# Performance work log

Measured on AMD Instinct MI355X. Metric: run time of the kernel, lower is better.

The kernel has to match this reference:

```python
import jax, jax.numpy as jnp
import numpy as np


def setup_inputs() -> dict:
    key = jax.random.key(0)
    k1, k2 = jax.random.split(key)
    N = 8192
    means = jax.random.normal(k1, (N, 3), dtype=jnp.float32) * 2.0
    normals = jax.random.normal(k2, (N, 3), dtype=jnp.float32)
    normals = normals / (jnp.linalg.norm(normals, axis=-1, keepdims=True) + 1e-8)
    return {"means": means, "normals": normals, "k": 8}


def reference(means, normals, k):
    # Pairwise Euclidean distances via the ||a-b||^2 expansion: avoids the
    # N x N x 3 diff tensor the original torch code materializes (same math).
    sq = jnp.sum(means * means, axis=-1)                      # (N,)
    d2 = sq[:, None] + sq[None, :] - 2.0 * (means @ means.T)  # (N, N)
    dists = jnp.sqrt(jnp.maximum(d2, 0.0))
    # k+1 smallest distances (self is the 0-distance nearest); drop self.
    dists = jax.lax.stop_gradient(dists)
    _, idx = jax.lax.top_k(-dists, k + 1)                     # (N, k+1)
    idx = idx[:, 1:]                                          # (N, k)
    neighbors = means[idx]                                    # (N, k, 3)
    local_diff = neighbors - means[:, None, :]                # (N, k, 3)
    plane_dist = jnp.sum(local_diff * normals[:, None, :], axis=-1)  # (N, k)
    return jnp.mean(jnp.abs(plane_dist))
```

## Files before the change

### kernel.cpp

```cpp
#include <hip/hip_runtime.h>
#include <hip/hip_bf16.h>

#define NPTS 8192
#define KNN 8
#define RPB 16
#define STAGES 8
#define SCOLS 1024

typedef __attribute__((ext_vector_type(8))) short bf16x8;
typedef __attribute__((ext_vector_type(4))) float f32x4;

__device__ __forceinline__ unsigned int bf16rne(float v) {
    unsigned int u = __float_as_uint(v);
    return (u + 0x7FFFu + ((u >> 16) & 1u)) >> 16;
}
__device__ __forceinline__ float bf2f(unsigned int h) { return __uint_as_float(h << 16); }

__device__ __forceinline__ void insert8(unsigned int (&best)[KNN], unsigned int key) {
#pragma unroll
    for (int t = 0; t < KNN; ++t) {
        const unsigned int lo = min(best[t], key);
        key = max(best[t], key);
        best[t] = lo;
    }
}
__device__ __forceinline__ void insert4(unsigned int (&b)[4], unsigned int key) {
#pragma unroll
    for (int t = 0; t < 4; ++t) {
        const unsigned int lo = min(b[t], key);
        key = max(b[t], key);
        b[t] = lo;
    }
}

__global__ __launch_bounds__(512) void prep_thresh(const float* __restrict__ means,
                                                   float4* __restrict__ pts,
                                                   uint4* __restrict__ cf0,
                                                   uint4* __restrict__ cf1,
                                                   uint4* __restrict__ rf0,
                                                   uint4* __restrict__ rf1,
                                                   float* __restrict__ Tm_arr,
                                                   float* __restrict__ out) {
    __shared__ unsigned int lds4[16][32][5];
    __shared__ unsigned int lds8[4][32][8];
    const int tid = threadIdx.x;
    const int pl = tid & 31;
    const int cls = tid >> 5;
    const int pt = blockIdx.x * 32 + pl;
    if (blockIdx.x == 0 && tid == 0) out[0] = 0.0f;

    const float x = means[3 * pt + 0];
    const float y = means[3 * pt + 1];
    const float z = means[3 * pt + 2];
    const float sq = x * x + y * y + z * z;
    if (cls == 0) {
        pts[pt] = make_float4(x, y, z, sq);
        const unsigned int hx = bf16rne(x), lx = bf16rne(x - bf2f(hx));
        const unsigned int hy = bf16rne(y), ly = bf16rne(y - bf2f(hy));
        const unsigned int hz = bf16rne(z), lz = bf16rne(z - bf2f(hz));
        const unsigned int hs = bf16rne(sq), ls = bf16rne(sq - bf2f(hs));
        cf0[pt] = make_uint4(hx | (lx << 16), hx | (hy << 16),
                             ly | (hy << 16), hz | (lz << 16));
        cf1[pt] = make_uint4(hz | (hs << 16), ls | (0x3F80u << 16), 0x3F80u, 0u);
        const float ax = -2.0f * x, ay = -2.0f * y, az = -2.0f * z;
        const unsigned int hax = bf16rne(ax), lax = bf16rne(ax - bf2f(hax));
        const unsigned int hay = bf16rne(ay), lay = bf16rne(ay - bf2f(hay));
        const unsigned int haz = bf16rne(az), laz = bf16rne(az - bf2f(haz));
        const unsigned int hsr = bf16rne(sq), lsr = bf16rne(sq - bf2f(hsr));
        rf0[pt] = make_uint4(hax | (hax << 16), lax | (hay << 16),
                             hay | (lay << 16), haz | (haz << 16));
        rf1[pt] = make_uint4(laz | (0x3F80u << 16), 0x3F80u | (hsr << 16), lsr, 0u);
    }

    const float mx2 = -2.0f * x, my2 = -2.0f * y, mz2 = -2.0f * z;
    unsigned int b4[4] = {~0u, ~0u, ~0u, ~0u};
#pragma unroll 4
    for (int m = 0; m < 32; ++m) {
        const int col = 16 * (cls + 16 * m);
        const float qx = means[3 * col + 0];
        const float qy = means[3 * col + 1];
        const float qz = means[3 * col + 2];
        const float qsq = qx * qx + qy * qy + qz * qz;
        const float d2 = fmaxf(fmaf(mx2, qx, fmaf(my2, qy, fmaf(mz2, qz, sq + qsq))), 0.0f);
        unsigned int key = (__float_as_uint(d2) & 0xFFFFE000u) | (unsigned int)col;
        key = (col == pt) ? ~0u : key;
        insert4(b4, key);
    }
#pragma unroll
    for (int j = 0; j < 4; ++j) lds4[cls][pl][j] = b4[j];
    __syncthreads();
    if (tid < 128) {
        const int p2 = tid & 31, q = tid >> 5;
        unsigned int bb[KNN];
#pragma unroll
        for (int s = 0; s < KNN; ++s) bb[s] = ~0u;
        for (int c = q * 4; c < q * 4 + 4; ++c)
#pragma unroll
            for (int j = 0; j < 4; ++j) insert8(bb, lds4[c][p2][j]);
#pragma unroll
        for (int s = 0; s < KNN; ++s) lds8[q][p2][s] = bb[s];
    }
    __syncthreads();
    if (tid < 32) {
        unsigned int bb[KNN];
#pragma unroll
        for (int s = 0; s < KNN; ++s) bb[s] = ~0u;
        for (int q = 0; q < 4; ++q)
#pragma unroll
            for (int s = 0; s < KNN; ++s) insert8(bb, lds8[q][tid][s]);
        const float Tf = __uint_as_float(bb[7] & 0xFFFFE000u);
        Tm_arr[blockIdx.x * 32 + tid] = Tf + 0.02f + 2e-3f * Tf;
    }
}

__global__ __launch_bounds__(512) void mfma_knn(const uint4* __restrict__ cf0,
                                                const uint4* __restrict__ cf1,
                                                const uint4* __restrict__ rf0,
                                                const uint4* __restrict__ rf1,
                                                const float4* __restrict__ pts,
                                                const float* __restrict__ Tm_arr,
                                                const float* __restrict__ normals,
                                                float* __restrict__ out) {
    __shared__ unsigned int lds_acc[8][16][64];
    __shared__ unsigned int km[8][RPB][KNN + 1];
    const int tid = threadIdx.x;
    const int l = tid & 63;
    const int wv = __builtin_amdgcn_readfirstlane(tid >> 6);
    const int R = l & 15;
    const int g = l >> 4;
    const int arow = blockIdx.x * RPB + R;

    const float4 mp = pts[arow];
    const float Tm = Tm_arr[arow];

    uint4 bu = make_uint4(0u, 0u, 0u, 0u);
    if (g == 0) bu = rf0[arow];
    else if (g == 1) bu = rf1[arow];
    union { uint4 u; bf16x8 v; } Bf; Bf.u = bu;
    const f32x4 zero = {0.0f, 0.0f, 0.0f, 0.0f};

    const uint4* __restrict__ asel = (g == 1) ? cf1 : cf0;

    unsigned int best[KNN];
#pragma unroll
    for (int s = 0; s < KNN; ++s) best[s] = ~0u;

#pragma unroll 1
    for (int s = 0; s < STAGES; ++s) {
        const int lbase = s * SCOLS + wv * 128 + R;
        const int cbase = s * SCOLS + wv * 128;
#pragma unroll
        for (int h = 0; h < 2; ++h) {
            unsigned int m = 0u;
#pragma unroll
            for (int mt4 = 0; mt4 < 4; ++mt4) {
                const int mt = h * 4 + mt4;
                union { uint4 u; bf16x8 v; } Af;
                Af.u = asel[lbase + mt * 16];
                const f32x4 acc = __builtin_amdgcn_mfma_f32_16x16x32_bf16(Af.v, Bf.v, zero, 0, 0, 0);
                lds_acc[wv][mt4 * 4 + 0][l] = __float_as_uint(acc[0]);
                lds_acc[wv][mt4 * 4 + 1][l] = __float_as_uint(acc[1]);
                lds_acc[wv][mt4 * 4 + 2][l] = __float_as_uint(acc[2]);
                lds_acc[wv][mt4 * 4 + 3][l] = __float_as_uint(acc[3]);
                m = m + m + ((acc[0] <= Tm) ? 1u : 0u);
                m = m + m + ((acc[1] <= Tm) ? 1u : 0u);
                m = m + m + ((acc[2] <= Tm) ? 1u : 0u);
                m = m + m + ((acc[3] <= Tm) ? 1u : 0u);
            }
            while (m) {
                const int b = __ffs(m) - 1;
                m &= m - 1;
                const int t = 15 - b;
                const float av = fmaxf(__uint_as_float(lds_acc[wv][t][l]), 0.0f);
                const int col = cbase + (h * 4 + (t >> 2)) * 16 + g * 4 + (t & 3);
                unsigned int key = (__float_as_uint(av) & 0xFFFFE000u) | (unsigned int)col;
                key = (col == arow) ? ~0u : key;
                insert8(best, key);
            }
        }
    }

#pragma unroll
    for (int st = 16; st <= 32; st <<= 1) {
        unsigned int tk[KNN];
#pragma unroll
        for (int s = 0; s < KNN; ++s) tk[s] = __shfl_xor(best[s], st);
#pragma unroll
        for (int s = 0; s < KNN; ++s) insert8(best, tk[s]);
    }
    if (l < RPB) {
#pragma unroll
        for (int s = 0; s < KNN; ++s) km[wv][l][s] = best[s];
    }
    for (int st = 1; st < 8; st <<= 1) {
        __syncthreads();
        if (((wv & (2 * st - 1)) == 0) && l < RPB) {
#pragma unroll
            for (int s = 0; s < KNN; ++s) insert8(best, km[wv + st][l][s]);
#pragma unroll
            for (int s = 0; s < KNN; ++s) km[wv][l][s] = best[s];
        }
    }

    if (wv == 0) {
        float sum = 0.0f;
        if (l < RPB) {
            const float nx = normals[3 * arow + 0];
            const float ny = normals[3 * arow + 1];
            const float nz = normals[3 * arow + 2];
#pragma unroll
            for (int s = 0; s < KNN; ++s) {
                const int nbr = (int)(best[s] & 0x1FFFu);
                const float4 q = pts[nbr];
                sum += fabsf((q.x - mp.x) * nx + (q.y - mp.y) * ny + (q.z - mp.z) * nz);
            }
        }
#pragma unroll
        for (int off = 8; off > 0; off >>= 1) sum += __shfl_down(sum, off);
        if (l == 0) atomicAdd(out, sum * (1.0f / ((float)NPTS * (float)KNN)));
    }
}

extern "C" void kernel_launch(void* const* d_in, const int* in_sizes, int n_in,
                              void* d_out, int out_size, void* d_ws, size_t ws_size,
                              hipStream_t stream) {
    const float* means = (const float*)d_in[0];
    const float* normals = (const float*)d_in[1];
    float* out = (float*)d_out;
    char* ws = (char*)d_ws;
    uint4* cf0 = (uint4*)ws;
    uint4* cf1 = (uint4*)(ws + 131072);
    uint4* rf0 = (uint4*)(ws + 262144);
    uint4* rf1 = (uint4*)(ws + 393216);
    float4* pts = (float4*)(ws + 524288);
    float* Tm = (float*)(ws + 655360);

    prep_thresh<<<NPTS / 32, 512, 0, stream>>>(means, pts, cf0, cf1, rf0, rf1, Tm, out);
    mfma_knn<<<NPTS / RPB, 512, 0, stream>>>(cf0, cf1, rf0, rf1, pts, Tm, normals, out);
}
```

Baseline: 36.98 us.

## Compute pruning threshold inside kNN kernel from an MFMA pre-pass stage

```diff
diff --git a/kernel.cpp b/kernel.cpp
--- a/kernel.cpp
+++ b/kernel.cpp
@@ -24,93 +24,44 @@
         best[t] = lo;
     }
 }
-__device__ __forceinline__ void insert4(unsigned int (&b)[4], unsigned int key) {
-#pragma unroll
-    for (int t = 0; t < 4; ++t) {
-        const unsigned int lo = min(b[t], key);
-        key = max(b[t], key);
+__device__ __forceinline__ void finsert8(float (&b)[KNN], float key) {
+#pragma unroll
+    for (int t = 0; t < KNN; ++t) {
+        const float lo = fminf(b[t], key);
+        key = fmaxf(b[t], key);
         b[t] = lo;
     }
 }
 
-__global__ __launch_bounds__(512) void prep_thresh(const float* __restrict__ means,
+__global__ __launch_bounds__(256) void pack_kernel(const float* __restrict__ means,
                                                    float4* __restrict__ pts,
                                                    uint4* __restrict__ cf0,
                                                    uint4* __restrict__ cf1,
                                                    uint4* __restrict__ rf0,
                                                    uint4* __restrict__ rf1,
-                                                   float* __restrict__ Tm_arr,
                                                    float* __restrict__ out) {
-    __shared__ unsigned int lds4[16][32][5];
-    __shared__ unsigned int lds8[4][32][8];
-    const int tid = threadIdx.x;
-    const int pl = tid & 31;
-    const int cls = tid >> 5;
-    const int pt = blockIdx.x * 32 + pl;
-    if (blockIdx.x == 0 && tid == 0) out[0] = 0.0f;
-
-    const float x = means[3 * pt + 0];
-    const float y = means[3 * pt + 1];
-    const float z = means[3 * pt + 2];
+    const int i = blockIdx.x * 256 + threadIdx.x;
+    if (i == 0) out[0] = 0.0f;
+    const float x = means[3 * i + 0];
+    const float y = means[3 * i + 1];
+    const float z = means[3 * i + 2];
     const float sq = x * x + y * y + z * z;
-    if (cls == 0) {
-        pts[pt] = make_float4(x, y, z, sq);
-        const unsigned int hx = bf16rne(x), lx = bf16rne(x - bf2f(hx));
-        const unsigned int hy = bf16rne(y), ly = bf16rne(y - bf2f(hy));
-        const unsigned int hz = bf16rne(z), lz = bf16rne(z - bf2f(hz));
-        const unsigned int hs = bf16rne(sq), ls = bf16rne(sq - bf2f(hs));
-        cf0[pt] = make_uint4(hx | (lx << 16), hx | (hy << 16),
-                             ly | (hy << 16), hz | (lz << 16));
-        cf1[pt] = make_uint4(hz | (hs << 16), ls | (0x3F80u << 16), 0x3F80u, 0u);
-        const float ax = -2.0f * x, ay = -2.0f * y, az = -2.0f * z;
-        const unsigned int hax = bf16rne(ax), lax = bf16rne(ax - bf2f(hax));
-        const unsigned int hay = bf16rne(ay), lay = bf16rne(ay - bf2f(hay));
-        const unsigned int haz = bf16rne(az), laz = bf16rne(az - bf2f(haz));
-        const unsigned int hsr = bf16rne(sq), lsr = bf16rne(sq - bf2f(hsr));
-        rf0[pt] = make_uint4(hax | (hax << 16), lax | (hay << 16),
-                             hay | (lay << 16), haz | (haz << 16));
-        rf1[pt] = make_uint4(laz | (0x3F80u << 16), 0x3F80u | (hsr << 16), lsr, 0u);
-    }
-
-    const float mx2 = -2.0f * x, my2 = -2.0f * y, mz2 = -2.0f * z;
-    unsigned int b4[4] = {~0u, ~0u, ~0u, ~0u};
-#pragma unroll 4
-    for (int m = 0; m < 32; ++m) {
-        const int col = 16 * (cls + 16 * m);
-        const float qx = means[3 * col + 0];
-        const float qy = means[3 * col + 1];
-        const float qz = means[3 * col + 2];
-        const float qsq = qx * qx + qy * qy + qz * qz;
-        const float d2 = fmaxf(fmaf(mx2, qx, fmaf(my2, qy, fmaf(mz2, qz, sq + qsq))), 0.0f);
-        unsigned int key = (__float_as_uint(d2) & 0xFFFFE000u) | (unsigned int)col;
-        key = (col == pt) ? ~0u : key;
-        insert4(b4, key);
-    }
-#pragma unroll
-    for (int j = 0; j < 4; ++j) lds4[cls][pl][j] = b4[j];
-    __syncthreads();
-    if (tid < 128) {
-        const int p2 = tid & 31, q = tid >> 5;
-        unsigned int bb[KNN];
-#pragma unroll
-        for (int s = 0; s < KNN; ++s) bb[s] = ~0u;
-        for (int c = q * 4; c < q * 4 + 4; ++c)
-#pragma unroll
-            for (int j = 0; j < 4; ++j) insert8(bb, lds4[c][p2][j]);
-#pragma unroll
-        for (int s = 0; s < KNN; ++s) lds8[q][p2][s] = bb[s];
-    }
-    __syncthreads();
-    if (tid < 32) {
-        unsigned int bb[KNN];
-#pragma unroll
-        for (int s = 0; s < KNN; ++s) bb[s] = ~0u;
-        for (int q = 0; q < 4; ++q)
-#pragma unroll
-            for (int s = 0; s < KNN; ++s) insert8(bb, lds8[q][tid][s]);
-        const float Tf = __uint_as_float(bb[7] & 0xFFFFE000u);
-        Tm_arr[blockIdx.x * 32 + tid] = Tf + 0.02f + 2e-3f * Tf;
-    }
+    pts[i] = make_float4(x, y, z, sq);
+    const unsigned int hx = bf16rne(x), lx = bf16rne(x - bf2f(hx));
+    const unsigned int hy = bf16rne(y), ly = bf16rne(y - bf2f(hy));
+    const unsigned int hz = bf16rne(z), lz = bf16rne(z - bf2f(hz));
+    const unsigned int hs = bf16rne(sq), ls = bf16rne(sq - bf2f(hs));
+    cf0[i] = make_uint4(hx | (lx << 16), hx | (hy << 16),
+                        ly | (hy << 16), hz | (lz << 16));
+    cf1[i] = make_uint4(hz | (hs << 16), ls | (0x3F80u << 16), 0x3F80u, 0u);
+    const float ax = -2.0f * x, ay = -2.0f * y, az = -2.0f * z;
+    const unsigned int hax = bf16rne(ax), lax = bf16rne(ax - bf2f(hax));
+    const unsigned int hay = bf16rne(ay), lay = bf16rne(ay - bf2f(hay));
+    const unsigned int haz = bf16rne(az), laz = bf16rne(az - bf2f(haz));
+    const unsigned int hsr = bf16rne(sq), lsr = bf16rne(sq - bf2f(hsr));
+    rf0[i] = make_uint4(hax | (hax << 16), lax | (hay << 16),
+                        hay | (lay << 16), haz | (haz << 16));
+    rf1[i] = make_uint4(laz | (0x3F80u << 16), 0x3F80u | (hsr << 16), lsr, 0u);
 }
 
 __global__ __launch_bounds__(512) void mfma_knn(const uint4* __restrict__ cf0,
@@ -118,10 +69,11 @@
                                                 const uint4* __restrict__ rf0,
                                                 const uint4* __restrict__ rf1,
                                                 const float4* __restrict__ pts,
-                                                const float* __restrict__ Tm_arr,
                                                 const float* __restrict__ normals,
                                                 float* __restrict__ out) {
     __shared__ unsigned int lds_acc[8][16][64];
+    __shared__ float lds_min[16][33];
+    __shared__ float lds_T[16];
     __shared__ unsigned int km[8][RPB][KNN + 1];
     const int tid = threadIdx.x;
     const int l = tid & 63;
@@ -131,7 +83,6 @@
     const int arow = blockIdx.x * RPB + R;
 
     const float4 mp = pts[arow];
-    const float Tm = Tm_arr[arow];
 
     uint4 bu = make_uint4(0u, 0u, 0u, 0u);
     if (g == 0) bu = rf0[arow];
@@ -140,6 +91,40 @@
     const f32x4 zero = {0.0f, 0.0f, 0.0f, 0.0f};
 
     const uint4* __restrict__ asel = (g == 1) ? cf1 : cf0;
+
+    const int sp = (((int)blockIdx.x >> 6) + 1) & 7;
+    {
+        const int lbase = sp * SCOLS + wv * 128 + R;
+        float lmin = 3.4e38f;
+#pragma unroll
+        for (int mt = 0; mt < 8; ++mt) {
+            union { uint4 u; bf16x8 v; } Af;
+            Af.u = asel[lbase + mt * 16];
+            const f32x4 acc = __builtin_amdgcn_mfma_f32_16x16x32_bf16(Af.v, Bf.v, zero, 0, 0, 0);
+            lmin = fminf(lmin, fminf(fminf(acc[0], acc[1]), fminf(acc[2], acc[3])));
+        }
+        lds_min[R][wv * 4 + g] = lmin;
+    }
+    __syncthreads();
+    {
+        const int row = wv * 2 + (l >> 5);
+        float bb[KNN];
+        bb[0] = lds_min[row][l & 31];
+#pragma unroll
+        for (int s = 1; s < KNN; ++s) bb[s] = 3.4e38f;
+#pragma unroll
+        for (int st = 1; st <= 16; st <<= 1) {
+            float tk[KNN];
+#pragma unroll
+            for (int s = 0; s < KNN; ++s) tk[s] = __shfl_xor(bb[s], st);
+#pragma unroll
+            for (int s = 0; s < KNN; ++s) finsert8(bb, tk[s]);
+        }
+        if ((l & 31) == 0)
+            lds_T[row] = bb[7] + 0.002f * fabsf(bb[7]) + 1e-5f;
+    }
+    __syncthreads();
+    const float Tm = lds_T[R];
 
     unsigned int best[KNN];
 #pragma unroll
@@ -233,8 +218,7 @@
     uint4* rf0 = (uint4*)(ws + 262144);
     uint4* rf1 = (uint4*)(ws + 393216);
     float4* pts = (float4*)(ws + 524288);
-    float* Tm = (float*)(ws + 655360);
-
-    prep_thresh<<<NPTS / 32, 512, 0, stream>>>(means, pts, cf0, cf1, rf0, rf1, Tm, out);
-    mfma_knn<<<NPTS / RPB, 512, 0, stream>>>(cf0, cf1, rf0, rf1, pts, Tm, normals, out);
-}
+
+    pack_kernel<<<NPTS / 256, 256, 0, stream>>>(means, pts, cf0, cf1, rf0, rf1, out);
+    mfma_knn<<<NPTS / RPB, 512, 0, stream>>>(cf0, cf1, rf0, rf1, pts, normals, out);
+}
```

Result: slower. 38.73 us (+4.7%).
